# Kernel optimization log

Hardware: AMD Instinct MI355X
Metric: run time of the kernel (lower is better)

The kernel has to match this reference:

```python
import jax, jax.numpy as jnp
import numpy as np

N_NODES = 50000
N_EDGES = 1600000
IN_DIM = 6
HID = 128
OUT = 128
N_LAYERS = 3
N_EXPERTS = 4
N_GRAPHS = 16
LOGN_SCALE = float(np.log(1e4))  # normalizes log(graph size) into ~[0,1]


def setup_inputs() -> dict:
    key = jax.random.key(0)
    ks = jax.random.split(key, 10)
    x = jax.random.normal(ks[0], (N_NODES, IN_DIM), dtype=jnp.float32)
    edge_index = jax.random.randint(ks[1], (2, N_EDGES), 0, N_NODES, dtype=jnp.int64)
    batch = jnp.sort(jax.random.randint(ks[2], (N_NODES,), 0, N_GRAPHS, dtype=jnp.int64))
    s = 1.0 / np.sqrt(HID)
    W_enc = jax.random.normal(ks[3], (IN_DIM, HID), dtype=jnp.float32) / np.sqrt(IN_DIM)
    b_enc = jnp.zeros((HID,), dtype=jnp.float32)
    # per-expert, per-layer GraphConv weights (hidden->hidden ... hidden->out; dims equal here)
    W_self = jax.random.normal(ks[4], (N_EXPERTS, N_LAYERS, HID, OUT), dtype=jnp.float32) * s
    W_nbr = jax.random.normal(ks[5], (N_EXPERTS, N_LAYERS, HID, OUT), dtype=jnp.float32) * s
    b_conv = jnp.zeros((N_EXPERTS, N_LAYERS, OUT), dtype=jnp.float32)
    centers = jnp.linspace(0.0, 1.0, N_EXPERTS, dtype=jnp.float32)
    return {"x": x, "edge_index": edge_index, "batch": batch, "W_enc": W_enc,
            "b_enc": b_enc, "W_self": W_self, "W_nbr": W_nbr, "b_conv": b_conv,
            "centers": centers}


def _expert(h, src, dst, Ws, Wn, b):
    # Ws, Wn: [L, H, H]; b: [L, H]
    for l in range(N_LAYERS):
        agg = jax.ops.segment_sum(h[src], dst, num_segments=N_NODES)  # gather+scatter
        h = h @ Ws[l] + agg @ Wn[l] + b[l]
        if l < N_LAYERS - 1:
            h = jax.nn.relu(h)
    return h


def reference(x, edge_index, batch, W_enc, b_enc, W_self, W_nbr, b_conv, centers):
    src, dst = edge_index[0], edge_index[1]
    h = jax.nn.relu(x @ W_enc + b_enc)  # SharedBusEncoder
    # graph size features: normalized log(#nodes per graph), per node
    counts = jax.ops.segment_sum(jnp.ones((N_NODES,), jnp.float32), batch,
                                 num_segments=N_GRAPHS)
    logn = jnp.log(jnp.maximum(counts, 1.0))[batch] / LOGN_SCALE  # [N]
    probs = jax.nn.softmax(-(logn[:, None] - centers[None, :]) ** 2, axis=-1)  # [N, E]
    y = jax.vmap(_expert, in_axes=(None, None, None, 0, 0, 0))(
        h, src, dst, W_self, W_nbr, b_conv)  # [E, N, OUT]
    return jnp.einsum('enh,ne->nh', y, probs)
```

## Files before the change

kernel.cpp:

```cpp
#include <hip/hip_runtime.h>

#define NN 50000
#define NE 1600000
#define NG 16
#define HID 128
#define NEXP 4
#define LOGN_SCALE 9.210340371976184f

#define NBUK 256
#define NPB  196
#define NBLK 64
#define EPB  ((NE + NBLK - 1)/NBLK)
#define MAXB 16384

typedef unsigned short u16;
typedef unsigned int u32;
typedef unsigned char u8;
typedef __attribute__((ext_vector_type(8))) short short8b;
typedef __attribute__((ext_vector_type(4))) float f32x4;
typedef __attribute__((ext_vector_type(2))) float f32x2;

static __device__ __forceinline__ float bf2f(u16 u){
  union { u32 i; float f; } c; c.i = ((u32)u)<<16; return c.f;
}
static __device__ __forceinline__ u16 f2bf(float f){
  union { float f; u32 i; } c; c.f = f;
  return (u16)((c.i + 0x7fffu + ((c.i>>16)&1u)) >> 16);
}
static __device__ __forceinline__ u8 f2fp8(float v){
  return (u8)(__builtin_amdgcn_cvt_pk_fp8_f32(v, v, 0, false) & 0xffu);
}

__global__ void k_bounds(const int* __restrict__ batch, int* __restrict__ gstart){
  int g = threadIdx.x;
  if(g > NG) return;
  int lo = 0, hi = NN;
  while(lo < hi){ int mid = (lo+hi)>>1; if(batch[mid] < g) lo = mid+1; else hi = mid; }
  gstart[g] = lo;
}

__global__ void k_probs(const int* __restrict__ batch, const int* __restrict__ gstart,
                        const float* __restrict__ centers, float* __restrict__ probs){
  int n = blockIdx.x*blockDim.x + threadIdx.x;
  if(n >= NN) return;
  int b = batch[n];
  float c = (float)(gstart[b+1] - gstart[b]);
  float logn = logf(fmaxf(c, 1.f)) * (1.f/LOGN_SCALE);
  float s[NEXP]; float m = -1e30f;
  #pragma unroll
  for(int e=0;e<NEXP;e++){ float d = logn - centers[e]; s[e] = -d*d; m = fmaxf(m, s[e]); }
  float sum = 0.f;
  #pragma unroll
  for(int e=0;e<NEXP;e++){ s[e] = expf(s[e]-m); sum += s[e]; }
  float inv = 1.f/sum;
  #pragma unroll
  for(int e=0;e<NEXP;e++) probs[n*NEXP+e] = s[e]*inv;
}

__global__ void k_enc(const float* __restrict__ x, const float* __restrict__ Wenc,
                      const float* __restrict__ benc, u16* __restrict__ h0,
                      u8* __restrict__ h08, float esc){
  int t = blockIdx.x*blockDim.x + threadIdx.x;
  if(t >= NN*HID) return;
  int n = t >> 7, j = t & 127;
  float acc = benc[j];
  #pragma unroll
  for(int k=0;k<6;k++) acc += x[n*6+k]*Wenc[k*HID+j];
  float v = fmaxf(acc, 0.f);
  h0[t] = f2bf(v);
  h08[t] = f2fp8(v*esc);
}

__global__ void k_wcvtT(const float* __restrict__ Wself, const float* __restrict__ Wnbr,
                        u16* __restrict__ WbfT){
  int t = blockIdx.x*blockDim.x + threadIdx.x;
  if(t >= 12*HID*256) return;
  int el = t / (HID*256);
  int r  = t % (HID*256);
  int j  = r >> 8;
  int k  = r & 255;
  float v = (k < HID) ? Wself[(size_t)el*HID*HID + (size_t)k*HID + j]
                      : Wnbr [(size_t)el*HID*HID + (size_t)(k-HID)*HID + j];
  WbfT[t] = f2bf(v);
}

__global__ __launch_bounds__(256) void k_hist(const int* __restrict__ dst,
                                              int* __restrict__ hist){
  __shared__ int h[NBUK];
  for(int i=threadIdx.x; i<NBUK; i+=256) h[i] = 0;
  __syncthreads();
  int e0 = blockIdx.x*EPB, e1 = min(NE, e0 + EPB);
  for(int e = e0 + (int)threadIdx.x; e < e1; e += 256)
    atomicAdd(&h[dst[e]/NPB], 1);
  __syncthreads();
  for(int i=threadIdx.x; i<NBUK; i+=256) hist[blockIdx.x*NBUK + i] = h[i];
}

__global__ __launch_bounds__(1024) void k_hscan(const int* __restrict__ hist,
                                                int* __restrict__ hoff,
                                                int* __restrict__ bbase){
  __shared__ int sd[NBLK*NBUK];
  __shared__ int ps[1024];
  int t = threadIdx.x;
  #pragma unroll
  for(int i=0;i<16;i++){
    int idx = t*16+i;
    sd[idx] = hist[(idx & (NBLK-1))*NBUK + (idx >> 6)];
  }
  __syncthreads();
  int sum = 0, base = t*16;
  #pragma unroll
  for(int i=0;i<16;i++){ int v = sd[base+i]; sd[base+i] = sum; sum += v; }
  ps[t] = sum;
  __syncthreads();
  for(int d=1; d<1024; d<<=1){
    int v = (t>=d) ? ps[t-d] : 0;
    __syncthreads();
    ps[t] += v;
    __syncthreads();
  }
  int add = (t>0) ? ps[t-1] : 0;
  #pragma unroll
  for(int i=0;i<16;i++){
    int idx = t*16+i;
    int bucket = idx>>6, blk = idx & (NBLK-1);
    int v = sd[idx] + add;
    hoff[blk*NBUK + bucket] = v;
    if(blk == 0) bbase[bucket] = v;
  }
  if(t == 1023) bbase[NBUK] = NE;
}

__global__ __launch_bounds__(256) void k_scatter(const int* __restrict__ src,
                                                 const int* __restrict__ dst,
                                                 const int* __restrict__ hoff,
                                                 u32* __restrict__ packed){
  __shared__ u32 cur[NBUK];
  for(int i=threadIdx.x; i<NBUK; i+=256) cur[i] = (u32)hoff[blockIdx.x*NBUK + i];
  __syncthreads();
  int e0 = blockIdx.x*EPB, e1 = min(NE, e0 + EPB);
  for(int e = e0 + (int)threadIdx.x; e < e1; e += 256){
    int d = dst[e];
    int b = d/NPB;
    u32 p = atomicAdd(&cur[b], 1u);
    packed[p] = (u32)src[e] | ((u32)(d - b*NPB) << 16);
  }
}

__global__ __launch_bounds__(256) void k_build(const u32* __restrict__ packed,
                                               const int* __restrict__ bbase,
                                               int* __restrict__ offs,
                                               u16* __restrict__ srcs16){
  __shared__ u32 ent[MAXB];
  __shared__ u16 outb[MAXB];
  __shared__ u32 cnt[256], exc[256], cur[256];
  int b = blockIdx.x, t = threadIdx.x;
  int e0 = bbase[b], e1 = bbase[b+1];
  int len = e1 - e0, cap = min(len, MAXB);
  for(int i=t; i<cap; i+=256) ent[i] = packed[e0+i];
  cnt[t] = 0;
  __syncthreads();
  for(int i=t; i<len; i+=256){
    u32 v = (i < MAXB) ? ent[i] : packed[e0+i];
    atomicAdd(&cnt[v>>16], 1u);
  }
  __syncthreads();
  u32 c = cnt[t];
  exc[t] = c;
  __syncthreads();
  for(int d=1; d<256; d<<=1){
    u32 v = (t>=(u32)d) ? exc[t-d] : 0u;
    __syncthreads();
    exc[t] += v;
    __syncthreads();
  }
  u32 excl = exc[t] - c;
  int node = b*NPB + t;
  if(t < NPB && node < NN) offs[node] = e0 + (int)excl;
  cur[t] = excl;
  if(b == NBUK-1 && t == 0) offs[NN] = NE;
  __syncthreads();
  for(int i=t; i<len; i+=256){
    u32 v = (i < MAXB) ? ent[i] : packed[e0+i];
    u32 p = atomicAdd(&cur[v>>16], 1u);
    u16 sv = (u16)(v & 0xffffu);
    if(p < (u32)MAXB) outb[p] = sv;
    else srcs16[e0+p] = sv;
  }
  __syncthreads();
  for(int i=t; i<cap; i+=256) srcs16[e0+i] = outb[i];
}

template<int BPL>
__global__ __launch_bounds__(256) void k_agg8(const u8* __restrict__ hin,
                                              const int* __restrict__ offs,
                                              const u16* __restrict__ srcs,
                                              u16* __restrict__ hout, float inv_scale){
  const int W = BPL*64;
  int node = blockIdx.x*4 + (threadIdx.x>>6);
  if(node >= NN) return;
  int lane = threadIdx.x & 63;
  const u8* hbase = hin + lane*BPL;
  float acc[BPL];
  #pragma unroll
  for(int i=0;i<BPL;i++) acc[i] = 0.f;
  int beg = offs[node], end = offs[node+1];
  for(int eb=beg; eb<end; eb+=64){
    int idx = eb + lane;
    int s = (idx < end) ? (int)srcs[idx] : 0;
    int cnt = min(64, end-eb);
    int j = 0;
    if(BPL == 8){
      for(; j+8<=cnt; j+=8){
        uint2 v[8];
        #pragma unroll
        for(int u=0;u<8;u++){
          int sj = __shfl(s, j+u, 64);
          v[u] = *(const uint2*)(hbase + (size_t)sj*W);
        }
        #pragma unroll
        for(int u=0;u<8;u++){
          f32x2 f0 = __builtin_amdgcn_cvt_pk_f32_fp8(v[u].x, false);
          f32x2 f1 = __builtin_amdgcn_cvt_pk_f32_fp8(v[u].x, true);
          f32x2 f2 = __builtin_amdgcn_cvt_pk_f32_fp8(v[u].y, false);
          f32x2 f3 = __builtin_amdgcn_cvt_pk_f32_fp8(v[u].y, true);
          acc[0]+=f0.x; acc[1]+=f0.y; acc[2]+=f1.x; acc[3]+=f1.y;
          acc[4]+=f2.x; acc[5]+=f2.y; acc[6]+=f3.x; acc[7]+=f3.y;
        }
      }
      for(; j<cnt; j++){
        int sj = __shfl(s, j, 64);
        uint2 v = *(const uint2*)(hbase + (size_t)sj*W);
        f32x2 f0 = __builtin_amdgcn_cvt_pk_f32_fp8(v.x, false);
        f32x2 f1 = __builtin_amdgcn_cvt_pk_f32_fp8(v.x, true);
        f32x2 f2 = __builtin_amdgcn_cvt_pk_f32_fp8(v.y, false);
        f32x2 f3 = __builtin_amdgcn_cvt_pk_f32_fp8(v.y, true);
        acc[0]+=f0.x; acc[1]+=f0.y; acc[2]+=f1.x; acc[3]+=f1.y;
        acc[4]+=f2.x; acc[5]+=f2.y; acc[6]+=f3.x; acc[7]+=f3.y;
      }
    } else {
      for(; j+8<=cnt; j+=8){
        u32 v[8];
        #pragma unroll
        for(int u=0;u<8;u++){
          int sj = __shfl(s, j+u, 64);
          v[u] = *(const u16*)(hbase + (size_t)sj*W);
        }
        #pragma unroll
        for(int u=0;u<8;u++){
          f32x2 f0 = __builtin_amdgcn_cvt_pk_f32_fp8(v[u], false);
          acc[0]+=f0.x; acc[1]+=f0.y;
        }
      }
      for(; j<cnt; j++){
        int sj = __shfl(s, j, 64);
        u32 v = *(const u16*)(hbase + (size_t)sj*W);
        f32x2 f0 = __builtin_amdgcn_cvt_pk_f32_fp8(v, false);
        acc[0]+=f0.x; acc[1]+=f0.y;
      }
    }
  }
  u16* o = hout + (size_t)node*W + lane*BPL;
  #pragma unroll
  for(int i=0;i<BPL;i++) o[i] = f2bf(acc[i]*inv_scale);
}

#define RPB 256
template<bool RELU>
__global__ __launch_bounds__(256) void k_gemm_mfma(
    const u16* __restrict__ hin, const u16* __restrict__ aggin,
    int in_stride, int in_eoff,
    const u16* __restrict__ WbfT, const float* __restrict__ bconv,
    int layer, u16* __restrict__ hout, u8* __restrict__ hout8, float enc8)
{
  int e = blockIdx.y;
  int wave = threadIdx.x >> 6, lane = threadIdx.x & 63;
  int l16 = lane & 15, lq = lane >> 4;
  int c0 = wave*32;
  const u16* WT = WbfT + (size_t)((e*3+layer)*HID)*256;

  short8b Bf[2][8];
  #pragma unroll
  for(int ct=0; ct<2; ct++){
    const u16* wp = WT + (size_t)(c0 + ct*16 + l16)*256 + lq*8;
    #pragma unroll
    for(int ks=0; ks<8; ks++)
      Bf[ct][ks] = *(const short8b*)(wp + ks*32);
  }
  const float* bias = bconv + (e*3+layer)*HID;
  float b0 = bias[c0 + l16], b1 = bias[c0 + 16 + l16];

  int nbase = blockIdx.x * RPB;
  #pragma unroll 1
  for(int it=0; it<RPB/32; it++){
    int n0 = nbase + it*32;
    if(n0 >= NN) break;
    f32x4 acc[2][2];
    #pragma unroll
    for(int rt=0; rt<2; rt++){
      acc[rt][0] = (f32x4){b0,b0,b0,b0};
      acc[rt][1] = (f32x4){b1,b1,b1,b1};
    }
    #pragma unroll
    for(int ks=0; ks<8; ks++){
      #pragma unroll
      for(int rt=0; rt<2; rt++){
        int n = n0 + rt*16 + l16;
        if(n > NN-1) n = NN-1;
        const u16* base = (ks < 4)
            ? (hin   + (size_t)n*in_stride + (size_t)e*in_eoff)
            : (aggin + (size_t)n*in_stride + (size_t)e*in_eoff - 128);
        short8b Af = *(const short8b*)(base + ks*32 + lq*8);
        acc[rt][0] = __builtin_amdgcn_mfma_f32_16x16x32_bf16(Af, Bf[0][ks], acc[rt][0], 0,0,0);
        acc[rt][1] = __builtin_amdgcn_mfma_f32_16x16x32_bf16(Af, Bf[1][ks], acc[rt][1], 0,0,0);
      }
    }
    #pragma unroll
    for(int rt=0; rt<2; rt++){
      int rowb = n0 + rt*16 + lq*4;
      #pragma unroll
      for(int r=0; r<4; r++){
        int n = rowb + r;
        if(n < NN){
          float v0 = acc[rt][0][r], v1 = acc[rt][1][r];
          if(RELU){ v0 = fmaxf(v0, 0.f); v1 = fmaxf(v1, 0.f); }
          u16* op = hout + (size_t)n*(NEXP*HID) + e*HID;
          op[c0 + l16]      = f2bf(v0);
          op[c0 + 16 + l16] = f2bf(v1);
          if(hout8){
            u8* op8 = hout8 + (size_t)n*(NEXP*HID) + e*HID;
            op8[c0 + l16]      = f2fp8(v0*enc8);
            op8[c0 + 16 + l16] = f2fp8(v1*enc8);
          }
        }
      }
    }
  }
}

__global__ void k_combine(const u16* __restrict__ y, const float* __restrict__ probs,
                          float* __restrict__ out){
  int t = blockIdx.x*blockDim.x + threadIdx.x;
  if(t >= NN*HID) return;
  int n = t >> 7, j = t & 127;
  const u16* yp = y + (size_t)n*(NEXP*HID);
  const float* pp = probs + n*NEXP;
  float r = pp[0]*bf2f(yp[j]) + pp[1]*bf2f(yp[HID+j])
          + pp[2]*bf2f(yp[2*HID+j]) + pp[3]*bf2f(yp[3*HID+j]);
  out[t] = r;
}

extern "C" void kernel_launch(void* const* d_in, const int* in_sizes, int n_in,
                              void* d_out, int out_size, void* d_ws, size_t ws_size,
                              hipStream_t stream){
  const float* x      = (const float*)d_in[0];
  const int*   eidx   = (const int*)d_in[1];
  const int*   batch  = (const int*)d_in[2];
  const float* Wenc   = (const float*)d_in[3];
  const float* benc   = (const float*)d_in[4];
  const float* Wself  = (const float*)d_in[5];
  const float* Wnbr   = (const float*)d_in[6];
  const float* bconv  = (const float*)d_in[7];
  const float* centers= (const float*)d_in[8];
  float* out = (float*)d_out;
  const int* src = eidx;
  const int* dst = eidx + NE;

  char* w = (char*)d_ws;
  size_t off = 0;
  auto alloc = [&](size_t b)->char*{ char* p = w + off; off = (off + b + 255) & ~(size_t)255; return p; };

  u16* h0    = (u16*)alloc((size_t)NN*HID*2);
  u16* agg0  = (u16*)alloc((size_t)NN*HID*2);
  u16* hA    = (u16*)alloc((size_t)NN*NEXP*HID*2);
  u16* hB    = (u16*)alloc((size_t)NN*NEXP*HID*2);
  u16* agg   = (u16*)alloc((size_t)NN*NEXP*HID*2);
  u16* WbfT  = (u16*)alloc((size_t)12*HID*256*2);
  u8*  h08   = (u8*)alloc((size_t)NN*HID);
  u8*  hA8   = (u8*)alloc((size_t)NN*NEXP*HID);
  float* probs = (float*)alloc((size_t)NN*NEXP*4);
  int* gstart = (int*)alloc(256);
  int* offs  = (int*)alloc((size_t)(NN+1)*4);
  u32* packed= (u32*)alloc((size_t)NE*4);
  u16* srcs16= (u16*)alloc((size_t)NE*2);
  int* hist  = (int*)alloc((size_t)NBLK*NBUK*4);
  int* hoff  = (int*)alloc((size_t)NBLK*NBUK*4);
  int* bbase = (int*)alloc((size_t)(NBUK+1)*4);
  if(off > ws_size) return;
  u8* hB8 = (u8*)h0;

  k_bounds<<<1, 32, 0, stream>>>(batch, gstart);
  k_probs<<<(NN+255)/256, 256, 0, stream>>>(batch, gstart, centers, probs);
  k_enc<<<(NN*HID+255)/256, 256, 0, stream>>>(x, Wenc, benc, h0, h08, 0.5f);
  k_wcvtT<<<(12*HID*256+255)/256, 256, 0, stream>>>(Wself, Wnbr, WbfT);

  k_hist<<<NBLK, 256, 0, stream>>>(dst, hist);
  k_hscan<<<1, 1024, 0, stream>>>(hist, hoff, bbase);
  k_scatter<<<NBLK, 256, 0, stream>>>(src, dst, hoff, packed);
  k_build<<<NBUK, 256, 0, stream>>>(packed, bbase, offs, srcs16);

  dim3 ggrid((NN + RPB - 1)/RPB, NEXP);

  k_agg8<2><<<(NN+3)/4, 256, 0, stream>>>(h08, offs, srcs16, agg0, 2.0f);
  k_gemm_mfma<true><<<ggrid, 256, 0, stream>>>(h0, agg0, HID, 0, WbfT, bconv, 0,
                                               hA, hA8, 1.f/16.f);
  k_agg8<8><<<(NN+3)/4, 256, 0, stream>>>(hA8, offs, srcs16, agg, 16.f);
  k_gemm_mfma<true><<<ggrid, 256, 0, stream>>>(hA, agg, NEXP*HID, HID, WbfT, bconv, 1,
                                               hB, hB8, 1.f/32.f);
  k_agg8<8><<<(NN+3)/4, 256, 0, stream>>>(hB8, offs, srcs16, agg, 32.f);
  k_gemm_mfma<false><<<ggrid, 256, 0, stream>>>(hB, agg, NEXP*HID, HID, WbfT, bconv, 2,
                                                hA, (u8*)nullptr, 0.f);

  k_combine<<<(NN*HID+255)/256, 256, 0, stream>>>(hA, probs, out);
}
```

Measured before the change: 641.4 us.

## Locally sort edges by bucket in LDS before coalesced global scatter

The edge scatter kernel now counts buckets per block, prefix-sums them, and reorders edges in shared memory by bucket. It then writes each bucket's run contiguously to global memory, instead of issuing random atomic-indexed global writes. The number of scatter blocks doubles and the histogram scan is adapted to match. This costs large shared-memory buffers per block, which lowers occupancy, plus extra scan work.

```diff
diff --git a/kernel.cpp b/kernel.cpp
--- a/kernel.cpp
+++ b/kernel.cpp
@@ -9,7 +9,7 @@
 
 #define NBUK 256
 #define NPB  196
-#define NBLK 64
+#define NBLK 128
 #define EPB  ((NE + NBLK - 1)/NBLK)
 #define MAXB 16384
 
@@ -102,15 +102,15 @@
   __shared__ int sd[NBLK*NBUK];
   __shared__ int ps[1024];
   int t = threadIdx.x;
-  #pragma unroll
-  for(int i=0;i<16;i++){
-    int idx = t*16+i;
-    sd[idx] = hist[(idx & (NBLK-1))*NBUK + (idx >> 6)];
-  }
-  __syncthreads();
-  int sum = 0, base = t*16;
-  #pragma unroll
-  for(int i=0;i<16;i++){ int v = sd[base+i]; sd[base+i] = sum; sum += v; }
+  for(int i=t; i<NBLK*NBUK; i+=1024){
+    int bucket = i >> 7;
+    int blk = i & (NBLK-1);
+    sd[i] = hist[blk*NBUK + bucket];
+  }
+  __syncthreads();
+  int base = t*32, sum = 0;
+  #pragma unroll
+  for(int i=0;i<32;i++){ int v = sd[base+i]; sd[base+i] = sum; sum += v; }
   ps[t] = sum;
   __syncthreads();
   for(int d=1; d<1024; d<<=1){
@@ -120,11 +120,9 @@
     __syncthreads();
   }
   int add = (t>0) ? ps[t-1] : 0;
-  #pragma unroll
-  for(int i=0;i<16;i++){
-    int idx = t*16+i;
-    int bucket = idx>>6, blk = idx & (NBLK-1);
-    int v = sd[idx] + add;
+  for(int i=base; i<base+32; i++){
+    int bucket = i >> 7, blk = i & (NBLK-1);
+    int v = sd[i] + add;
     hoff[blk*NBUK + bucket] = v;
     if(blk == 0) bbase[bucket] = v;
   }
@@ -135,15 +133,46 @@
                                                  const int* __restrict__ dst,
                                                  const int* __restrict__ hoff,
                                                  u32* __restrict__ packed){
-  __shared__ u32 cur[NBUK];
-  for(int i=threadIdx.x; i<NBUK; i+=256) cur[i] = (u32)hoff[blockIdx.x*NBUK + i];
-  __syncthreads();
-  int e0 = blockIdx.x*EPB, e1 = min(NE, e0 + EPB);
-  for(int e = e0 + (int)threadIdx.x; e < e1; e += 256){
-    int d = dst[e];
-    int b = d/NPB;
-    u32 p = atomicAdd(&cur[b], 1u);
-    packed[p] = (u32)src[e] | ((u32)(d - b*NPB) << 16);
+  __shared__ u32 ent[EPB];
+  __shared__ u32 outp[EPB];
+  __shared__ u32 cnt[NBUK], exc[NBUK], cur[NBUK], gb[NBUK];
+  int t = threadIdx.x;
+  int e0 = blockIdx.x*EPB;
+  int len = min(EPB, NE - e0);
+  cnt[t] = 0;
+  __syncthreads();
+  for(int i=t; i<len; i+=256){
+    int d = dst[e0+i];
+    u32 b = (u32)(d/NPB);
+    ent[i] = (u32)src[e0+i] | ((u32)(d - (int)b*NPB) << 16) | (b << 24);
+    atomicAdd(&cnt[b], 1u);
+  }
+  __syncthreads();
+  u32 c = cnt[t];
+  exc[t] = c;
+  __syncthreads();
+  for(int d=1; d<256; d<<=1){
+    u32 v = (t>=(u32)d) ? exc[t-d] : 0u;
+    __syncthreads();
+    exc[t] += v;
+    __syncthreads();
+  }
+  u32 excl = exc[t] - c;
+  cur[t] = excl;
+  gb[t] = (u32)hoff[blockIdx.x*NBUK + t];
+  __syncthreads();
+  exc[t] = excl;
+  __syncthreads();
+  for(int i=t; i<len; i+=256){
+    u32 v = ent[i];
+    u32 p = atomicAdd(&cur[v>>24], 1u);
+    outp[p] = v;
+  }
+  __syncthreads();
+  for(int i=t; i<len; i+=256){
+    u32 v = outp[i];
+    u32 b = v >> 24;
+    packed[gb[b] + ((u32)i - exc[b])] = v & 0x00ffffffu;
   }
 }
 
@@ -162,7 +191,7 @@
   __syncthreads();
   for(int i=t; i<len; i+=256){
     u32 v = (i < MAXB) ? ent[i] : packed[e0+i];
-    atomicAdd(&cnt[v>>16], 1u);
+    atomicAdd(&cnt[(v>>16)&0xffu], 1u);
   }
   __syncthreads();
   u32 c = cnt[t];
@@ -182,7 +211,7 @@
   __syncthreads();
   for(int i=t; i<len; i+=256){
     u32 v = (i < MAXB) ? ent[i] : packed[e0+i];
-    u32 p = atomicAdd(&cur[v>>16], 1u);
+    u32 p = atomicAdd(&cur[(v>>16)&0xffu], 1u);
     u16 sv = (u16)(v & 0xffffu);
     if(p < (u32)MAXB) outb[p] = sv;
     else srcs16[e0+p] = sv;
```

Measured after the change: 611.9 us. 4.6% less time.
